# Performance work log

Hardware: AMD Instinct MI355X
Metric: run time of the kernel (lower is better)

Reference implementation:

```python
import jax, jax.numpy as jnp
import numpy as np

B, N, D, F = 4096, 64, 64, 4096
KP_DIM = N * (N + 1) // 2  # 2080
# static row-major triu/tril index lists (matches torch.masked_select ordering)
_TRIU_I, _TRIU_J = (np.array(a) for a in np.triu_indices(N, 0))
_TRIL_I, _TRIL_J = (np.array(a) for a in np.tril_indices(N, 0))


def setup_inputs() -> dict:
    key = jax.random.key(0)
    k1, k2, k3, k4 = jax.random.split(key, 4)
    feature_emb = jax.random.normal(k1, (B, N, D), dtype=jnp.float32)
    # xavier_normal for [D, D]
    std = float(np.sqrt(2.0 / (D + D)))
    kp_W = jax.random.normal(k2, (D, D), dtype=jnp.float32) * std
    # nn.Linear weights are [out_features, in_features]
    bound = float(1.0 / np.sqrt(KP_DIM))
    W_triu = jax.random.uniform(k3, (F, KP_DIM), dtype=jnp.float32, minval=-bound, maxval=bound)
    W_tril = jax.random.uniform(k4, (F, KP_DIM), dtype=jnp.float32, minval=-bound, maxval=bound)
    return {"feature_emb": feature_emb, "kp_W": kp_W, "W_triu": W_triu, "W_tril": W_tril}


def reference(feature_emb, kp_W, W_triu, W_tril):
    # embs_kp[b,i,j] = e[b,i,:] @ kp_W @ e[b,j,:]  -> [B, N, N]
    embs_kp = jnp.einsum("bnd,de,bme->bnm", feature_emb, kp_W, feature_emb)
    triu = embs_kp[:, _TRIU_I, _TRIU_J]  # [B, kp_dim], row-major order
    tril = embs_kp[:, _TRIL_I, _TRIL_J]  # [B, kp_dim]
    embs_flatten = feature_emb.reshape(feature_emb.shape[0], -1)  # [B, N*D]
    view_1 = triu @ W_triu.T  # [B, F]
    view_2 = tril @ W_tril.T  # [B, F]
    return (embs_flatten, view_1, view_2)
```

## Files before the change

kernel.cpp:

```cpp
#include <hip/hip_runtime.h>

typedef __bf16 bf16x8 __attribute__((ext_vector_type(8)));
typedef float f32x4 __attribute__((ext_vector_type(4)));
typedef unsigned short u16x4 __attribute__((ext_vector_type(4)));
typedef unsigned short u16x8 __attribute__((ext_vector_type(8)));

#define KP 2112
#define NT 33

__device__ __forceinline__ unsigned short f2bf(float f) {
  unsigned int u = __builtin_bit_cast(unsigned int, f);
  u += 0x7FFFu + ((u >> 16) & 1u);
  return (unsigned short)(u >> 16);
}

__device__ __forceinline__ bf16x8 ld_frag(const unsigned short* p) {
  return __builtin_bit_cast(bf16x8, *(const u16x8*)p);
}

#define MFMA16(a, b, c) __builtin_amdgcn_mfma_f32_16x16x32_bf16((a), (b), (c), 0, 0, 0)

__device__ __forceinline__ void cp16(const void* g, void* l) {
  __builtin_amdgcn_global_load_lds(
      (const __attribute__((address_space(1))) unsigned int*)g,
      (__attribute__((address_space(3))) unsigned int*)l, 16, 0, 0);
}

__device__ __forceinline__ void barrier_sync() {
  asm volatile("" ::: "memory");
  __builtin_amdgcn_s_barrier();
  __builtin_amdgcn_sched_barrier(0);
}

#define VMWAIT(N) asm volatile("s_waitcnt vmcnt(" #N ")" ::: "memory")

__global__ __launch_bounds__(256) void cvt_pad(const float* __restrict__ in,
                                               unsigned short* __restrict__ out) {
  const int total = 4096 * (KP / 4);
  int i = blockIdx.x * 256 + threadIdx.x;
  const int stride = gridDim.x * 256;
  for (; i < total; i += stride) {
    const int row = i / (KP / 4);
    const int c4 = i - row * (KP / 4);
    u16x4 o = {0, 0, 0, 0};
    if (c4 < 520) {
      float4 v = *(const float4*)(in + (size_t)row * 2080 + c4 * 4);
      o[0] = f2bf(v.x); o[1] = f2bf(v.y); o[2] = f2bf(v.z); o[3] = f2bf(v.w);
    }
    ((u16x4*)out)[i] = o;
  }
}

__global__ __launch_bounds__(256) void prep_wt(const float* __restrict__ W,
                                               unsigned short* __restrict__ Wt) {
  const int tid = threadIdx.x;
#pragma unroll
  for (int j = 0; j < 16; ++j) {
    const int o = tid * 16 + j;
    const int c = o >> 6, d = o & 63;
    Wt[o] = f2bf(W[d * 64 + c]);
  }
}

__global__ __launch_bounds__(256) void batch_kp(
    const float* __restrict__ E,
    const unsigned short* __restrict__ Wt,
    float* __restrict__ out0,
    unsigned short* __restrict__ triu,
    unsigned short* __restrict__ tril)
{
  __shared__ __align__(16) unsigned short sE[64 * 64];
  __shared__ __align__(16) unsigned short sWt[64 * 64];
  __shared__ __align__(16) unsigned short sT[64 * 64];

  const int b = blockIdx.x;
  const int tid = threadIdx.x;
  const float* Eb = E + (size_t)b * 4096;
  float* o0 = out0 + (size_t)b * 4096;

  cp16(Wt + tid * 8, sWt + tid * 8);
  cp16(Wt + 2048 + tid * 8, sWt + 2048 + tid * 8);

#pragma unroll
  for (int it = 0; it < 4; ++it) {
    const int flat = it * 1024 + tid * 4;
    float4 v = *(const float4*)(Eb + flat);
    *(float4*)(o0 + flat) = v;
    u16x4 e;
    e[0] = f2bf(v.x); e[1] = f2bf(v.y); e[2] = f2bf(v.z); e[3] = f2bf(v.w);
    *(u16x4*)(sE + flat) = e;
  }
  __syncthreads();

  const int lane = tid & 63, w = tid >> 6;
  const int fr = lane & 15;
  const int fk = (lane >> 4) << 3;
  const int qr = (lane >> 4) << 2;

#pragma unroll
  for (int ct = 0; ct < 4; ++ct) {
    f32x4 acc = {0.f, 0.f, 0.f, 0.f};
#pragma unroll
    for (int k2 = 0; k2 < 2; ++k2) {
      bf16x8 a = ld_frag(sE + (w * 16 + fr) * 64 + k2 * 32 + fk);
      bf16x8 bb = ld_frag(sWt + (ct * 16 + fr) * 64 + k2 * 32 + fk);
      acc = MFMA16(a, bb, acc);
    }
#pragma unroll
    for (int r = 0; r < 4; ++r)
      sT[(w * 16 + qr + r) * 64 + ct * 16 + fr] = f2bf(acc[r]);
  }
  __syncthreads();

  unsigned short* tu = triu + (size_t)b * KP;
  unsigned short* tl = tril + (size_t)b * KP;
  if (tid < 32) { tu[2080 + tid] = 0; tl[2080 + tid] = 0; }
#pragma unroll
  for (int ct = 0; ct < 4; ++ct) {
    f32x4 acc = {0.f, 0.f, 0.f, 0.f};
#pragma unroll
    for (int k2 = 0; k2 < 2; ++k2) {
      bf16x8 a = ld_frag(sT + (w * 16 + fr) * 64 + k2 * 32 + fk);
      bf16x8 bb = ld_frag(sE + (ct * 16 + fr) * 64 + k2 * 32 + fk);
      acc = MFMA16(a, bb, acc);
    }
#pragma unroll
    for (int r = 0; r < 4; ++r) {
      const int i = w * 16 + qr + r;
      const int j = ct * 16 + fr;
      const unsigned short v = f2bf(acc[r]);
      if (j >= i) tu[i * 64 - ((i * (i - 1)) >> 1) + (j - i)] = v;
      if (j <= i) tl[((i * (i + 1)) >> 1) + j] = v;
    }
  }
}

__global__ __launch_bounds__(512, 2) void gemm_views(
    const unsigned short* __restrict__ triu, const unsigned short* __restrict__ tril,
    const unsigned short* __restrict__ Wu, const unsigned short* __restrict__ Wl,
    float* __restrict__ dout)
{
  __shared__ __align__(16) unsigned short lds[65536];

  const int z = blockIdx.z;
  const unsigned short* Ag = z ? tril : triu;
  const unsigned short* Bg = z ? Wl : Wu;
  float* C = dout + (size_t)16777216 * (size_t)(1 + z);

  const int tid = threadIdx.x;
  const int lane = tid & 63, wv = tid >> 6;
  const int m0 = blockIdx.y << 8, n0 = blockIdx.x << 8;

  const int lr = lane >> 3;
  const int cuch = (lane & 7) ^ lr;
  const int rA = wv * 8 + lr;
  const int rB = (wv & 3) * 8 + (wv >> 2) * 64 + lr;
  const unsigned short* gA = Ag + (size_t)(m0 + rA) * KP + cuch * 8;
  const unsigned short* gB = Bg + (size_t)(n0 + rB) * KP + cuch * 8;
  const int dA = tid * 8;
  const int dB = (wv & 3) * 512 + (wv >> 2) * 4096 + lane * 8;

  const int fr = lane & 15, fq = lane >> 4;
  const int rowA0 = (wv >> 2) * 128 + fr;
  const int rowB0 = (wv & 3) * 64 + fr;

  f32x4 acc[8][4] = {};
  bf16x8 aA_[4], aB_[4], bA_[4], bB_[4];

#define STAGE_A(B_, KT, OFF) do { \
    cp16(gA + (size_t)(OFF) * KP + (KT) * 64, lds + (B_) * 32768 + (OFF) * 64 + dA); \
    cp16(gA + (size_t)((OFF) + 128) * KP + (KT) * 64, \
         lds + (B_) * 32768 + ((OFF) + 128) * 64 + dA); \
  } while (0)
#define STAGE_B(B_, KT, OFF) do { \
    cp16(gB + (size_t)(OFF) * KP + (KT) * 64, \
         lds + (B_) * 32768 + 16384 + (OFF) * 64 + dB); \
    cp16(gB + (size_t)((OFF) + 128) * KP + (KT) * 64, \
         lds + (B_) * 32768 + 16384 + ((OFF) + 128) * 64 + dB); \
  } while (0)
#define LDA(S, B_, MH, KH) do { _Pragma("unroll") \
    for (int mt = 0; mt < 4; ++mt) \
      S[mt] = ld_frag(lds + (B_) * 32768 + (rowA0 + (MH) * 64 + mt * 16) * 64 + \
                      ((((KH) * 4 + fq) ^ (fr & 7)) * 8)); \
  } while (0)
#define LDB(S, B_, KH) do { _Pragma("unroll") \
    for (int nt = 0; nt < 4; ++nt) \
      S[nt] = ld_frag(lds + (B_) * 32768 + 16384 + (rowB0 + nt * 16) * 64 + \
                      ((((KH) * 4 + fq) ^ (fr & 7)) * 8)); \
  } while (0)
#define PH_MFMA(AS, BS, MH) do { \
    __builtin_amdgcn_s_setprio(1); \
    _Pragma("unroll") for (int mt = 0; mt < 4; ++mt) \
    _Pragma("unroll") for (int nt = 0; nt < 4; ++nt) \
      acc[(MH) * 4 + mt][nt] = MFMA16(AS[mt], BS[nt], acc[(MH) * 4 + mt][nt]); \
    __builtin_amdgcn_s_setprio(0); \
  } while (0)

  STAGE_A(0, 0, 0);
  STAGE_B(0, 0, 0);
  STAGE_B(0, 0, 32);
  STAGE_A(0, 0, 64);
  STAGE_B(1, 1, 0);
  STAGE_B(1, 1, 32);
  STAGE_A(1, 1, 0);
  VMWAIT(6);
  barrier_sync();
  LDA(aB_, 0, 0, 0);
  LDB(bA_, 0, 0);

  for (int t = 0; t < NT; ++t) {
    const int cb = t & 1, nb = cb ^ 1;
    const int t1 = (t + 1 < NT) ? t + 1 : NT - 1;
    const int t2 = (t + 2 < NT) ? t + 2 : NT - 1;
    LDA(aA_, cb, 1, 0);
    STAGE_A(nb, t1, 64);
    barrier_sync();
    PH_MFMA(aB_, bA_, 0);
    barrier_sync();
    LDA(aB_, cb, 1, 1);
    LDB(bB_, cb, 1);
    barrier_sync();
    PH_MFMA(aA_, bA_, 1);
    barrier_sync();
    LDA(aA_, cb, 0, 1);
    STAGE_B(cb, t2, 0);
    barrier_sync();
    PH_MFMA(aB_, bB_, 1);
    VMWAIT(4);
    barrier_sync();
    LDA(aB_, nb, 0, 0);
    LDB(bA_, nb, 0);
    STAGE_B(cb, t2, 32);
    STAGE_A(cb, t2, 0);
    barrier_sync();
    PH_MFMA(aA_, bB_, 0);
    VMWAIT(6);
    barrier_sync();
  }

  const int qr = fq << 2;
  const int crow = m0 + (wv >> 2) * 128 + qr;
  const int ccol = n0 + (wv & 3) * 64 + fr;
#pragma unroll
  for (int mt = 0; mt < 8; ++mt)
#pragma unroll
    for (int nt = 0; nt < 4; ++nt) {
      float* cp = C + (size_t)(crow + mt * 16) * 4096 + (ccol + nt * 16);
#pragma unroll
      for (int r = 0; r < 4; ++r) cp[(size_t)r * 4096] = acc[mt][nt][r];
    }
#undef STAGE_A
#undef STAGE_B
#undef LDA
#undef LDB
#undef PH_MFMA
}

extern "C" void kernel_launch(void* const* d_in, const int* in_sizes, int n_in,
                              void* d_out, int out_size, void* d_ws, size_t ws_size,
                              hipStream_t stream) {
  const float* feat  = (const float*)d_in[0];
  const float* kpW   = (const float*)d_in[1];
  const float* Wtriu = (const float*)d_in[2];
  const float* Wtril = (const float*)d_in[3];
  float* out = (float*)d_out;

  const size_t per = (size_t)4096 * KP;
  unsigned short* triu_bf = (unsigned short*)d_ws;
  unsigned short* tril_bf = triu_bf + per;
  unsigned short* Wu_bf   = tril_bf + per;
  unsigned short* Wl_bf   = Wu_bf + per;
  unsigned short* Wt_bf   = Wl_bf + per;

  cvt_pad<<<dim3(1024), dim3(256), 0, stream>>>(Wtriu, Wu_bf);
  cvt_pad<<<dim3(1024), dim3(256), 0, stream>>>(Wtril, Wl_bf);
  prep_wt<<<dim3(1), dim3(256), 0, stream>>>(kpW, Wt_bf);
  batch_kp<<<dim3(4096), dim3(256), 0, stream>>>(feat, Wt_bf, out, triu_bf, tril_bf);
  gemm_views<<<dim3(16, 16, 2), dim3(512), 0, stream>>>(triu_bf, tril_bf, Wu_bf, Wl_bf, out);
}
```

Measured before the change: 426.5 us.

## Stage kp matrix in LDS for vectorized tri stores, trim GEMM barriers, merge prep kernels

batch_kp now writes the 64x64 bf16 product into shared memory and emits the packed upper and lower triangles as coalesced 16-byte stores, replacing scattered 2-byte global writes. Each thread recovers its starting (i,j) index with a sqrt estimate followed by correction loops. The GEMM main loop drops half its barriers, and barrier_sync now waits on lgkmcnt(0) so LDS fragment loads finish before each remaining barrier. The two cvt_pad launches are merged into one 2D launch and prep_wt is spread over 16 blocks; removing barriers risks LDS hazards between staging and fragment reads.

```diff
diff --git a/kernel.cpp b/kernel.cpp
--- a/kernel.cpp
+++ b/kernel.cpp
@@ -27,38 +27,72 @@
 }
 
 __device__ __forceinline__ void barrier_sync() {
-  asm volatile("" ::: "memory");
+  asm volatile("s_waitcnt lgkmcnt(0)" ::: "memory");
   __builtin_amdgcn_s_barrier();
   __builtin_amdgcn_sched_barrier(0);
 }
 
 #define VMWAIT(N) asm volatile("s_waitcnt vmcnt(" #N ")" ::: "memory")
 
-__global__ __launch_bounds__(256) void cvt_pad(const float* __restrict__ in,
-                                               unsigned short* __restrict__ out) {
-  const int total = 4096 * (KP / 4);
-  int i = blockIdx.x * 256 + threadIdx.x;
-  const int stride = gridDim.x * 256;
-  for (; i < total; i += stride) {
-    const int row = i / (KP / 4);
-    const int c4 = i - row * (KP / 4);
+__global__ __launch_bounds__(256) void cvt_pad(
+    const float* __restrict__ inu, const float* __restrict__ inl,
+    unsigned short* __restrict__ outu, unsigned short* __restrict__ outl) {
+  const float* in = blockIdx.y ? inl : inu;
+  unsigned short* out = blockIdx.y ? outl : outu;
+  const int row = blockIdx.x;
+  const float* src = in + (size_t)row * 2080;
+  unsigned short* dst = out + (size_t)row * KP;
+  for (int c = threadIdx.x; c < 528; c += 256) {
     u16x4 o = {0, 0, 0, 0};
-    if (c4 < 520) {
-      float4 v = *(const float4*)(in + (size_t)row * 2080 + c4 * 4);
+    if (c < 520) {
+      float4 v = *(const float4*)(src + c * 4);
       o[0] = f2bf(v.x); o[1] = f2bf(v.y); o[2] = f2bf(v.z); o[3] = f2bf(v.w);
     }
-    ((u16x4*)out)[i] = o;
+    ((u16x4*)dst)[c] = o;
   }
 }
 
 __global__ __launch_bounds__(256) void prep_wt(const float* __restrict__ W,
                                                unsigned short* __restrict__ Wt) {
-  const int tid = threadIdx.x;
-#pragma unroll
-  for (int j = 0; j < 16; ++j) {
-    const int o = tid * 16 + j;
-    const int c = o >> 6, d = o & 63;
-    Wt[o] = f2bf(W[d * 64 + c]);
+  const int o = blockIdx.x * 256 + threadIdx.x;
+  const int c = o >> 6, d = o & 63;
+  Wt[o] = f2bf(W[d * 64 + c]);
+}
+
+__device__ __forceinline__ void emit_tri(const unsigned short* __restrict__ sK,
+                                         unsigned short* __restrict__ dst,
+                                         bool upper, int tid) {
+#pragma unroll
+  for (int jj = 0; jj < 2; ++jj) {
+    if (jj == 1 && tid >= 8) break;
+    const int p0 = (jj == 0) ? tid * 8 : 2048 + tid * 8;
+    int i, j;
+    if (upper) {
+      float s = sqrtf(4160.25f - 2.0f * (float)p0);
+      i = (int)(64.5f - s);
+      if (i < 0) i = 0;
+      if (i > 63) i = 63;
+      while (i > 0 && i * (129 - i) / 2 > p0) --i;
+      while (i < 63 && (i + 1) * (128 - i) / 2 <= p0) ++i;
+      j = i + (p0 - i * (129 - i) / 2);
+    } else {
+      float s = sqrtf(8.0f * (float)p0 + 1.0f);
+      i = (int)((s - 1.0f) * 0.5f);
+      if (i < 0) i = 0;
+      if (i > 63) i = 63;
+      while (i > 0 && i * (i + 1) / 2 > p0) --i;
+      while (i < 63 && (i + 1) * (i + 2) / 2 <= p0) ++i;
+      j = p0 - i * (i + 1) / 2;
+    }
+    u16x8 o;
+#pragma unroll
+    for (int e = 0; e < 8; ++e) {
+      const int p = p0 + e;
+      o[e] = (p < 2080 && i < 64) ? sK[i * 64 + j] : (unsigned short)0;
+      if (upper) { if (++j > 63) { ++i; j = i; } }
+      else       { if (++j > i)  { ++i; j = 0; } }
+    }
+    *(u16x8*)(dst + p0) = o;
   }
 }
 
@@ -112,9 +146,7 @@
   }
   __syncthreads();
 
-  unsigned short* tu = triu + (size_t)b * KP;
-  unsigned short* tl = tril + (size_t)b * KP;
-  if (tid < 32) { tu[2080 + tid] = 0; tl[2080 + tid] = 0; }
+  unsigned short* sK = sWt;
 #pragma unroll
   for (int ct = 0; ct < 4; ++ct) {
     f32x4 acc = {0.f, 0.f, 0.f, 0.f};
@@ -125,14 +157,13 @@
       acc = MFMA16(a, bb, acc);
     }
 #pragma unroll
-    for (int r = 0; r < 4; ++r) {
-      const int i = w * 16 + qr + r;
-      const int j = ct * 16 + fr;
-      const unsigned short v = f2bf(acc[r]);
-      if (j >= i) tu[i * 64 - ((i * (i - 1)) >> 1) + (j - i)] = v;
-      if (j <= i) tl[((i * (i + 1)) >> 1) + j] = v;
-    }
-  }
+    for (int r = 0; r < 4; ++r)
+      sK[(w * 16 + qr + r) * 64 + ct * 16 + fr] = f2bf(acc[r]);
+  }
+  __syncthreads();
+
+  emit_tri(sK, triu + (size_t)b * KP, true, tid);
+  emit_tri(sK, tril + (size_t)b * KP, false, tid);
 }
 
 __global__ __launch_bounds__(512, 2) void gemm_views(
@@ -214,17 +245,14 @@
     const int t2 = (t + 2 < NT) ? t + 2 : NT - 1;
     LDA(aA_, cb, 1, 0);
     STAGE_A(nb, t1, 64);
-    barrier_sync();
     PH_MFMA(aB_, bA_, 0);
     barrier_sync();
     LDA(aB_, cb, 1, 1);
     LDB(bB_, cb, 1);
-    barrier_sync();
     PH_MFMA(aA_, bA_, 1);
     barrier_sync();
     LDA(aA_, cb, 0, 1);
     STAGE_B(cb, t2, 0);
-    barrier_sync();
     PH_MFMA(aB_, bB_, 1);
     VMWAIT(4);
     barrier_sync();
@@ -232,7 +260,6 @@
     LDB(bA_, nb, 0);
     STAGE_B(cb, t2, 32);
     STAGE_A(cb, t2, 0);
-    barrier_sync();
     PH_MFMA(aA_, bB_, 0);
     VMWAIT(6);
     barrier_sync();
@@ -272,9 +299,8 @@
   unsigned short* Wl_bf   = Wu_bf + per;
   unsigned short* Wt_bf   = Wl_bf + per;
 
-  cvt_pad<<<dim3(1024), dim3(256), 0, stream>>>(Wtriu, Wu_bf);
-  cvt_pad<<<dim3(1024), dim3(256), 0, stream>>>(Wtril, Wl_bf);
-  prep_wt<<<dim3(1), dim3(256), 0, stream>>>(kpW, Wt_bf);
+  cvt_pad<<<dim3(4096, 2), dim3(256), 0, stream>>>(Wtriu, Wtril, Wu_bf, Wl_bf);
+  prep_wt<<<dim3(16), dim3(256), 0, stream>>>(kpW, Wt_bf);
   batch_kp<<<dim3(4096), dim3(256), 0, stream>>>(feat, Wt_bf, out, triu_bf, tril_bf);
   gemm_views<<<dim3(16, 16, 2), dim3(512), 0, stream>>>(triu_bf, tril_bf, Wu_bf, Wl_bf, out);
 }
```

After: 428.4 us. About the same (+0.4%).
